# Kernel optimization log

Measured on AMD Instinct MI355X. Metric: run time of the kernel, lower is better.

The kernel has to match this reference:

```python
import jax, jax.numpy as jnp
import numpy as np

N_ENTITIES = 300000
N_ITEMS = 150000
N_USERS = 150000
N_EDGES = 2000000
N_INTER = 2000000
N_REL = 32
D = 64


def _scatter_mean(src, index, dim_size):
    # torch_scatter.scatter_mean: sum per segment divided by count; empty segments -> 0
    sums = jax.ops.segment_sum(src, index, num_segments=dim_size)
    cnt = jax.ops.segment_sum(jnp.ones((src.shape[0],), src.dtype), index, num_segments=dim_size)
    return sums / jnp.maximum(cnt, 1.0)[:, None]


def setup_inputs() -> dict:
    key = jax.random.key(0)
    ks = jax.random.split(key, 9)
    return {
        "entity_emb": jax.random.normal(ks[0], (N_ENTITIES, D), dtype=jnp.float32),
        "user_emb": jax.random.normal(ks[1], (N_USERS, D), dtype=jnp.float32),
        "edge_index": jax.random.randint(ks[2], (2, N_EDGES), 0, N_ENTITIES),
        "edge_type": jax.random.randint(ks[3], (N_EDGES,), 0, N_REL),
        "mat_row": jax.random.randint(ks[4], (N_INTER,), 0, N_USERS),
        "mat_col": jax.random.randint(ks[5], (N_INTER,), 0, N_ITEMS),
        "weight": jax.random.normal(ks[6], (N_REL, D), dtype=jnp.float32),
        "gate1_w": jax.random.normal(ks[7], (D, D), dtype=jnp.float32) * 0.1,
        "gate2_w": jax.random.normal(ks[8], (D, D), dtype=jnp.float32) * 0.1,
    }


def reference(entity_emb, user_emb, edge_index, edge_type, mat_row, mat_col, weight, gate1_w, gate2_w):
    head, tail = edge_index[0], edge_index[1]
    # KG aggregation: gather tail embeddings, modulate by relation emb, scatter-mean to head
    neigh_relation_emb = entity_emb[tail] * weight[edge_type]          # [E, D]
    entity_kg_agg = _scatter_mean(neigh_relation_emb, head, N_ENTITIES)
    item_kg_agg = entity_kg_agg[:N_ITEMS]                              # [I, D]
    att_kg_agg = entity_kg_agg[N_ITEMS:]                               # [Ent-I, D]
    # interaction aggregation: gather user emb by row, scatter-mean to item (col)
    item_int_agg = _scatter_mean(user_emb[mat_row], mat_col, N_ITEMS)  # [I, D]
    # gated fusion (F.linear: x @ W.T)
    gi = jax.nn.sigmoid(item_kg_agg @ gate1_w.T + item_int_agg @ gate2_w.T)
    item_emb_fusion = gi * item_kg_agg + (1.0 - gi) * item_int_agg
    # sparse mm with all-ones values == segment sum of fused item embs over users
    user_agg = jax.ops.segment_sum(item_emb_fusion[mat_col], mat_row, num_segments=N_USERS)
    final_entity_agg = jnp.concatenate([item_emb_fusion, att_kg_agg], axis=0)
    return (final_entity_agg, user_agg, item_kg_agg, item_int_agg)
```

## Files before the change

### kernel.cpp

```cpp
#include <hip/hip_runtime.h>

#define N_ENTITIES 300000
#define N_ITEMS    150000
#define N_USERS    150000
#define N_EDGES    2000000
#define N_INTER    2000000
#define D          64
#define N_TOT      (N_ENTITIES + N_ITEMS + N_USERS)

__global__ void hist_rank_kernel(const int* __restrict__ head,
                                 const int* __restrict__ mat_col,
                                 const int* __restrict__ mat_row,
                                 int* __restrict__ cnt,
                                 int* __restrict__ r_ent,
                                 int* __restrict__ r_item,
                                 int* __restrict__ r_user) {
    int e = blockIdx.x * 256 + threadIdx.x;
    if (e >= N_EDGES) return;
    int h = head[e], c = mat_col[e], r = mat_row[e];
    int a0 = atomicAdd(&cnt[h], 1);
    int a1 = atomicAdd(&cnt[N_ENTITIES + c], 1);
    int a2 = atomicAdd(&cnt[N_ENTITIES + N_ITEMS + r], 1);
    r_ent[e]  = a0;
    r_item[e] = a1;
    r_user[e] = a2;
}

__global__ void transpose_gates_kernel(const float* __restrict__ g1,
                                       const float* __restrict__ g2,
                                       float* __restrict__ g1t,
                                       float* __restrict__ g2t) {
    int i = blockIdx.x * 256 + threadIdx.x;
    if (i >= 64 * 64) return;
    int o = i >> 6, k = i & 63;
    g1t[k * 64 + o] = g1[i];
    g2t[k * 64 + o] = g2[i];
}

__global__ __launch_bounds__(256) void scan_partial(const int* __restrict__ in,
                                                    int* __restrict__ incl,
                                                    int* __restrict__ bsums,
                                                    int n) {
    __shared__ int lds[256];
    int t = threadIdx.x;
    int base = blockIdx.x * 1024 + t * 4;
    int v0 = (base + 0 < n) ? in[base + 0] : 0;
    int v1 = (base + 1 < n) ? in[base + 1] : 0;
    int v2 = (base + 2 < n) ? in[base + 2] : 0;
    int v3 = (base + 3 < n) ? in[base + 3] : 0;
    int s = v0 + v1 + v2 + v3;
    lds[t] = s;
    __syncthreads();
    for (int off = 1; off < 256; off <<= 1) {
        int x = (t >= off) ? lds[t - off] : 0;
        __syncthreads();
        lds[t] += x;
        __syncthreads();
    }
    int excl = lds[t] - s;
    if (base + 0 < n) incl[base + 0] = excl + v0;
    if (base + 1 < n) incl[base + 1] = excl + v0 + v1;
    if (base + 2 < n) incl[base + 2] = excl + v0 + v1 + v2;
    if (base + 3 < n) incl[base + 3] = excl + s;
    if (t == 255) bsums[blockIdx.x] = lds[255];
}

__global__ __launch_bounds__(1024) void scan_bsums(int* __restrict__ bsums, int nb) {
    __shared__ int lds[1024];
    int t = threadIdx.x;
    lds[t] = (t < nb) ? bsums[t] : 0;
    __syncthreads();
    for (int off = 1; off < 1024; off <<= 1) {
        int x = (t >= off) ? lds[t - off] : 0;
        __syncthreads();
        lds[t] += x;
        __syncthreads();
    }
    if (t < nb) bsums[t] = lds[t];
}

__global__ void scan_finalize(const int* __restrict__ incl,
                              const int* __restrict__ bsums,
                              int* __restrict__ off_ent,
                              int* __restrict__ off_item,
                              int* __restrict__ off_user) {
    int i = blockIdx.x * 256 + threadIdx.x;
    if (i >= N_TOT) return;
    int b = i >> 10;
    int g = incl[i] + ((b > 0) ? bsums[b - 1] : 0);
    if (i < N_ENTITIES) {
        off_ent[i + 1] = g;
        if (i == 0) { off_ent[0] = 0; }
    } else if (i < N_ENTITIES + N_ITEMS) {
        off_item[i - N_ENTITIES + 1] = g - N_EDGES;
        if (i == N_ENTITIES) { off_item[0] = 0; }
    } else {
        off_user[i - N_ENTITIES - N_ITEMS + 1] = g - 2 * N_EDGES;
        if (i == N_ENTITIES + N_ITEMS) { off_user[0] = 0; }
    }
}

__global__ void scatter_all_kernel(const int* __restrict__ head,
                                   const int* __restrict__ tail,
                                   const int* __restrict__ type,
                                   const int* __restrict__ mat_row,
                                   const int* __restrict__ mat_col,
                                   const int* __restrict__ r_ent,
                                   const int* __restrict__ r_item,
                                   const int* __restrict__ r_user,
                                   const int* __restrict__ off_ent,
                                   const int* __restrict__ off_item,
                                   const int* __restrict__ off_user,
                                   int* __restrict__ tt_sorted,
                                   int* __restrict__ row_sorted,
                                   int* __restrict__ col_sorted) {
    int e = blockIdx.x * 256 + threadIdx.x;
    if (e >= N_EDGES) return;
    int h = head[e], t = tail[e], ty = type[e];
    int r = mat_row[e], c = mat_col[e];
    tt_sorted[off_ent[h] + r_ent[e]]   = t | (ty << 19);
    row_sorted[off_item[c] + r_item[e]] = r;
    col_sorted[off_user[r] + r_user[e]] = c;
}

__global__ __launch_bounds__(256, 8) void agg_ent_kernel(
        const float* __restrict__ entity_emb, const float* __restrict__ weight,
        const int* __restrict__ off, const int* __restrict__ tt_sorted,
        float* __restrict__ out_item_kg, float* __restrict__ out_final) {
    int wave = threadIdx.x >> 6, lane = threadIdx.x & 63;
    int g = lane >> 4, q = lane & 15;
    int ent = blockIdx.x * 4 + wave;
    if (ent >= N_ENTITIES) return;
    int s = off[ent], e = off[ent + 1];
    int cnt = e - s;
    const float4* __restrict__ emb4 = (const float4*)entity_emb;
    const float4* __restrict__ wt4  = (const float4*)weight;
    float ax = 0.f, ay = 0.f, az = 0.f, aw = 0.f;
    for (int idx = s + g; idx < e; idx += 8) {
        int v0 = tt_sorted[idx];
        int i2 = idx + 4;
        bool p2 = (i2 < e);
        int v1 = p2 ? tt_sorted[i2] : 0;
        {
            int t = v0 & 0x7FFFF, w = v0 >> 19;
            float4 a = emb4[t * 16 + q];
            float4 b = wt4[w * 16 + q];
            ax += a.x * b.x; ay += a.y * b.y; az += a.z * b.z; aw += a.w * b.w;
        }
        if (p2) {
            int t = v1 & 0x7FFFF, w = v1 >> 19;
            float4 a = emb4[t * 16 + q];
            float4 b = wt4[w * 16 + q];
            ax += a.x * b.x; ay += a.y * b.y; az += a.z * b.z; aw += a.w * b.w;
        }
    }
    ax += __shfl_xor(ax, 16); ax += __shfl_xor(ax, 32);
    ay += __shfl_xor(ay, 16); ay += __shfl_xor(ay, 32);
    az += __shfl_xor(az, 16); az += __shfl_xor(az, 32);
    aw += __shfl_xor(aw, 16); aw += __shfl_xor(aw, 32);
    if (g == 0) {
        float inv = 1.0f / (float)(cnt > 1 ? cnt : 1);
        float4 r; r.x = ax * inv; r.y = ay * inv; r.z = az * inv; r.w = aw * inv;
        if (ent < N_ITEMS) ((float4*)out_item_kg)[ent * 16 + q] = r;
        else               ((float4*)out_final)[ent * 16 + q]   = r;
    }
}

__global__ __launch_bounds__(512, 6) void agg_item_fuse_kernel(
        const float* __restrict__ user_emb,
        const int* __restrict__ off, const int* __restrict__ row_sorted,
        const float* __restrict__ item_kg,
        const float* __restrict__ g1t, const float* __restrict__ g2t,
        float* __restrict__ out_item_int, float* __restrict__ out_final) {
    __shared__ float s_g1t[4096];
    __shared__ float s_g2t[4096];
    __shared__ float s_ii[8 * 64];

    {
        const float4* a = (const float4*)g1t;
        const float4* b = (const float4*)g2t;
        float4* sa = (float4*)s_g1t;
        float4* sb = (float4*)s_g2t;
        #pragma unroll
        for (int i = threadIdx.x; i < 1024; i += 512) { sa[i] = a[i]; sb[i] = b[i]; }
    }

    int wave = threadIdx.x >> 6, lane = threadIdx.x & 63;
    int g = lane >> 4, q = lane & 15;
    int item = blockIdx.x * 8 + wave;
    int s = off[item], e = off[item + 1];
    int cnt = e - s;
    const float4* __restrict__ ue4 = (const float4*)user_emb;
    float ax = 0.f, ay = 0.f, az = 0.f, aw = 0.f;
    for (int idx = s + g; idx < e; idx += 8) {
        int r0 = row_sorted[idx];
        int i2 = idx + 4;
        bool p2 = (i2 < e);
        int r1 = p2 ? row_sorted[i2] : 0;
        {
            float4 v = ue4[r0 * 16 + q];
            ax += v.x; ay += v.y; az += v.z; aw += v.w;
        }
        if (p2) {
            float4 v = ue4[r1 * 16 + q];
            ax += v.x; ay += v.y; az += v.z; aw += v.w;
        }
    }
    ax += __shfl_xor(ax, 16); ax += __shfl_xor(ax, 32);
    ay += __shfl_xor(ay, 16); ay += __shfl_xor(ay, 32);
    az += __shfl_xor(az, 16); az += __shfl_xor(az, 32);
    aw += __shfl_xor(aw, 16); aw += __shfl_xor(aw, 32);
    float inv = 1.0f / (float)(cnt > 1 ? cnt : 1);
    ax *= inv; ay *= inv; az *= inv; aw *= inv;
    if (g == 0) {
        float4 t; t.x = ax; t.y = ay; t.z = az; t.w = aw;
        *(float4*)&s_ii[wave * 64 + 4 * q] = t;
    }
    __syncthreads();

    const float* __restrict__ kgrow = item_kg + (long long)item * 64;
    float gx = 0.f, gy = 0.f, gz = 0.f, gw = 0.f;
    #pragma unroll 4
    for (int i = 0; i < 16; ++i) {
        int k = 16 * g + i;
        float kk = kgrow[k];
        float ik = s_ii[wave * 64 + k];
        float4 w1 = *(const float4*)&s_g1t[k * 64 + 4 * q];
        float4 w2 = *(const float4*)&s_g2t[k * 64 + 4 * q];
        gx += kk * w1.x + ik * w2.x;
        gy += kk * w1.y + ik * w2.y;
        gz += kk * w1.z + ik * w2.z;
        gw += kk * w1.w + ik * w2.w;
    }
    gx += __shfl_xor(gx, 16); gx += __shfl_xor(gx, 32);
    gy += __shfl_xor(gy, 16); gy += __shfl_xor(gy, 32);
    gz += __shfl_xor(gz, 16); gz += __shfl_xor(gz, 32);
    gw += __shfl_xor(gw, 16); gw += __shfl_xor(gw, 32);

    if (g == 0) {
        float4 kg4 = *(const float4*)&kgrow[4 * q];
        float4 ii4; ii4.x = ax; ii4.y = ay; ii4.z = az; ii4.w = aw;
        float4 o;
        float s0 = 1.0f / (1.0f + __expf(-gx)); o.x = s0 * kg4.x + (1.0f - s0) * ii4.x;
        float s1 = 1.0f / (1.0f + __expf(-gy)); o.y = s1 * kg4.y + (1.0f - s1) * ii4.y;
        float s2 = 1.0f / (1.0f + __expf(-gz)); o.z = s2 * kg4.z + (1.0f - s2) * ii4.z;
        float s3 = 1.0f / (1.0f + __expf(-gw)); o.w = s3 * kg4.w + (1.0f - s3) * ii4.w;
        ((float4*)out_item_int)[item * 16 + q] = ii4;
        ((float4*)out_final)[item * 16 + q]    = o;
    }
}

__global__ __launch_bounds__(256, 8) void agg_user_kernel(
        const float* __restrict__ fusion,
        const int* __restrict__ off, const int* __restrict__ col_sorted,
        float* __restrict__ out_user) {
    int wave = threadIdx.x >> 6, lane = threadIdx.x & 63;
    int g = lane >> 4, q = lane & 15;
    int user = blockIdx.x * 4 + wave;
    if (user >= N_USERS) return;
    int s = off[user], e = off[user + 1];
    const float4* __restrict__ f4 = (const float4*)fusion;
    float ax = 0.f, ay = 0.f, az = 0.f, aw = 0.f;
    for (int idx = s + g; idx < e; idx += 8) {
        int c0 = col_sorted[idx];
        int i2 = idx + 4;
        bool p2 = (i2 < e);
        int c1 = p2 ? col_sorted[i2] : 0;
        {
            float4 v = f4[c0 * 16 + q];
            ax += v.x; ay += v.y; az += v.z; aw += v.w;
        }
        if (p2) {
            float4 v = f4[c1 * 16 + q];
            ax += v.x; ay += v.y; az += v.z; aw += v.w;
        }
    }
    ax += __shfl_xor(ax, 16); ax += __shfl_xor(ax, 32);
    ay += __shfl_xor(ay, 16); ay += __shfl_xor(ay, 32);
    az += __shfl_xor(az, 16); az += __shfl_xor(az, 32);
    aw += __shfl_xor(aw, 16); aw += __shfl_xor(aw, 32);
    if (g == 0) {
        float4 r; r.x = ax; r.y = ay; r.z = az; r.w = aw;
        ((float4*)out_user)[user * 16 + q] = r;
    }
}


extern "C" void kernel_launch(void* const* d_in, const int* in_sizes, int n_in,
                              void* d_out, int out_size, void* d_ws, size_t ws_size,
                              hipStream_t stream) {
    const float* entity_emb = (const float*)d_in[0];
    const float* user_emb   = (const float*)d_in[1];
    const int*   edge_index = (const int*)d_in[2];
    const int*   edge_type  = (const int*)d_in[3];
    const int*   mat_row    = (const int*)d_in[4];
    const int*   mat_col    = (const int*)d_in[5];
    const float* weight     = (const float*)d_in[6];
    const float* g1         = (const float*)d_in[7];
    const float* g2         = (const float*)d_in[8];

    const int* edge_head = edge_index;
    const int* edge_tail = edge_index + N_EDGES;

    float* out = (float*)d_out;
    float* out_final    = out;
    float* out_user     = out + (long long)N_ENTITIES * D;
    float* out_item_kg  = out_user + (long long)N_USERS * D;
    float* out_item_int = out_item_kg + (long long)N_ITEMS * D;

    int* w = (int*)d_ws;
    float* g1t_glob = (float*)w;  w += 64 * 64;
    float* g2t_glob = (float*)w;  w += 64 * 64;
    int* cnt       = w;  w += N_TOT;
    int* off_ent   = w;  w += N_ENTITIES + 1;
    int* off_item  = w;  w += N_ITEMS + 1;
    int* off_user  = w;  w += N_USERS + 1;
    int* incl_tmp  = w;  w += N_TOT;
    int* bsums     = w;  w += 1024;
    int* r_ent     = w;  w += N_EDGES;
    int* r_item    = w;  w += N_INTER;
    int* r_user    = w;  w += N_INTER;
    int* tt_sorted = w;  w += N_EDGES;
    int* row_sorted= w;  w += N_INTER;
    int* col_sorted= w;  w += N_INTER;

    hipMemsetAsync(cnt, 0, (size_t)N_TOT * sizeof(int), stream);

    const int EB = (N_EDGES + 255) / 256;

    transpose_gates_kernel<<<16, 256, 0, stream>>>(g1, g2, g1t_glob, g2t_glob);

    hist_rank_kernel<<<EB, 256, 0, stream>>>(edge_head, mat_col, mat_row,
                                             cnt, r_ent, r_item, r_user);

    {
        int nb = (N_TOT + 1023) / 1024;
        scan_partial<<<nb, 256, 0, stream>>>(cnt, incl_tmp, bsums, N_TOT);
        scan_bsums<<<1, 1024, 0, stream>>>(bsums, nb);
        scan_finalize<<<(N_TOT + 255) / 256, 256, 0, stream>>>(
            incl_tmp, bsums, off_ent, off_item, off_user);
    }

    scatter_all_kernel<<<EB, 256, 0, stream>>>(
        edge_head, edge_tail, edge_type, mat_row, mat_col,
        r_ent, r_item, r_user, off_ent, off_item, off_user,
        tt_sorted, row_sorted, col_sorted);

    agg_ent_kernel<<<N_ENTITIES / 4, 256, 0, stream>>>(
        entity_emb, weight, off_ent, tt_sorted, out_item_kg, out_final);
    agg_item_fuse_kernel<<<N_ITEMS / 8, 512, 0, stream>>>(
        user_emb, off_item, row_sorted, out_item_kg, g1t_glob, g2t_glob,
        out_item_int, out_final);
    agg_user_kernel<<<N_USERS / 4, 256, 0, stream>>>(
        out_final, off_user, col_sorted, out_user);
}
```

Baseline: 1.027 ms.

## Privatize histogram counters per XCD to keep atomics local

Each XCD now atomically increments its own copy of the count array, selected by reading the hardware XCC id, instead of sharing one global array. This targets the cost of cross-die coherence traffic on atomics. The scan sums the eight copies, and a packed per-bin byte prefix tells the scatter where each XCD's slots begin. In exchange it adds eight times the memset and scan reads plus an extra prefix array. Packing offsets into 8 bits assumes no bin holds 256 or more items from one XCD.

```diff
diff --git a/kernel.cpp b/kernel.cpp
--- a/kernel.cpp
+++ b/kernel.cpp
@@ -7,23 +7,33 @@
 #define N_INTER    2000000
 #define D          64
 #define N_TOT      (N_ENTITIES + N_ITEMS + N_USERS)
+#define NXCD       8
+
+__device__ __forceinline__ int xcc_id() {
+    int x;
+    asm volatile("s_getreg_b32 %0, hwreg(HW_REG_XCC_ID)" : "=s"(x));
+    return x & (NXCD - 1);
+}
 
 __global__ void hist_rank_kernel(const int* __restrict__ head,
                                  const int* __restrict__ mat_col,
                                  const int* __restrict__ mat_row,
-                                 int* __restrict__ cnt,
+                                 int* __restrict__ cnt_x,
                                  int* __restrict__ r_ent,
                                  int* __restrict__ r_item,
                                  int* __restrict__ r_user) {
     int e = blockIdx.x * 256 + threadIdx.x;
     if (e >= N_EDGES) return;
+    int x = xcc_id();
+    int* __restrict__ mycnt = cnt_x + x * N_TOT;
+    int xt = x << 24;
     int h = head[e], c = mat_col[e], r = mat_row[e];
-    int a0 = atomicAdd(&cnt[h], 1);
-    int a1 = atomicAdd(&cnt[N_ENTITIES + c], 1);
-    int a2 = atomicAdd(&cnt[N_ENTITIES + N_ITEMS + r], 1);
-    r_ent[e]  = a0;
-    r_item[e] = a1;
-    r_user[e] = a2;
+    int a0 = atomicAdd(&mycnt[h], 1);
+    int a1 = atomicAdd(&mycnt[N_ENTITIES + c], 1);
+    int a2 = atomicAdd(&mycnt[N_ENTITIES + N_ITEMS + r], 1);
+    r_ent[e]  = a0 | xt;
+    r_item[e] = a1 | xt;
+    r_user[e] = a2 | xt;
 }
 
 __global__ void transpose_gates_kernel(const float* __restrict__ g1,
@@ -37,17 +47,22 @@
     g2t[k * 64 + o] = g2[i];
 }
 
-__global__ __launch_bounds__(256) void scan_partial(const int* __restrict__ in,
+__global__ __launch_bounds__(256) void scan_partial(const int* __restrict__ cnt_x,
                                                     int* __restrict__ incl,
                                                     int* __restrict__ bsums,
                                                     int n) {
     __shared__ int lds[256];
     int t = threadIdx.x;
     int base = blockIdx.x * 1024 + t * 4;
-    int v0 = (base + 0 < n) ? in[base + 0] : 0;
-    int v1 = (base + 1 < n) ? in[base + 1] : 0;
-    int v2 = (base + 2 < n) ? in[base + 2] : 0;
-    int v3 = (base + 3 < n) ? in[base + 3] : 0;
+    int v0 = 0, v1 = 0, v2 = 0, v3 = 0;
+    #pragma unroll
+    for (int x = 0; x < NXCD; ++x) {
+        const int* __restrict__ c = cnt_x + x * N_TOT;
+        if (base + 0 < n) v0 += c[base + 0];
+        if (base + 1 < n) v1 += c[base + 1];
+        if (base + 2 < n) v2 += c[base + 2];
+        if (base + 3 < n) v3 += c[base + 3];
+    }
     int s = v0 + v1 + v2 + v3;
     lds[t] = s;
     __syncthreads();
@@ -81,13 +96,27 @@
 
 __global__ void scan_finalize(const int* __restrict__ incl,
                               const int* __restrict__ bsums,
+                              const int* __restrict__ cnt_x,
                               int* __restrict__ off_ent,
                               int* __restrict__ off_item,
-                              int* __restrict__ off_user) {
+                              int* __restrict__ off_user,
+                              uint2* __restrict__ prefx) {
     int i = blockIdx.x * 256 + threadIdx.x;
     if (i >= N_TOT) return;
     int b = i >> 10;
     int g = incl[i] + ((b > 0) ? bsums[b - 1] : 0);
+
+    unsigned lo = 0, hi = 0;
+    int tot = 0;
+    #pragma unroll
+    for (int x = 0; x < NXCD; ++x) {
+        unsigned p = (unsigned)(tot & 0xFF);
+        if (x < 4) lo |= p << (8 * x);
+        else       hi |= p << (8 * (x - 4));
+        tot += cnt_x[x * N_TOT + i];
+    }
+    prefx[i] = make_uint2(lo, hi);
+
     if (i < N_ENTITIES) {
         off_ent[i + 1] = g;
         if (i == 0) { off_ent[0] = 0; }
@@ -98,6 +127,10 @@
         off_user[i - N_ENTITIES - N_ITEMS + 1] = g - 2 * N_EDGES;
         if (i == N_ENTITIES + N_ITEMS) { off_user[0] = 0; }
     }
+}
+
+__device__ __forceinline__ int pfx_get(uint2 p, int x) {
+    return (int)(((x < 4) ? (p.x >> (8 * x)) : (p.y >> (8 * (x - 4)))) & 0xFFu);
 }
 
 __global__ void scatter_all_kernel(const int* __restrict__ head,
@@ -111,6 +144,7 @@
                                    const int* __restrict__ off_ent,
                                    const int* __restrict__ off_item,
                                    const int* __restrict__ off_user,
+                                   const uint2* __restrict__ prefx,
                                    int* __restrict__ tt_sorted,
                                    int* __restrict__ row_sorted,
                                    int* __restrict__ col_sorted) {
@@ -118,9 +152,17 @@
     if (e >= N_EDGES) return;
     int h = head[e], t = tail[e], ty = type[e];
     int r = mat_row[e], c = mat_col[e];
-    tt_sorted[off_ent[h] + r_ent[e]]   = t | (ty << 19);
-    row_sorted[off_item[c] + r_item[e]] = r;
-    col_sorted[off_user[r] + r_user[e]] = c;
+
+    int v0 = r_ent[e];
+    int v1 = r_item[e];
+    int v2 = r_user[e];
+    int p0 = pfx_get(prefx[h], v0 >> 24);
+    int p1 = pfx_get(prefx[N_ENTITIES + c], v1 >> 24);
+    int p2 = pfx_get(prefx[N_ENTITIES + N_ITEMS + r], v2 >> 24);
+
+    tt_sorted[off_ent[h]  + p0 + (v0 & 0xFFFFFF)] = t | (ty << 19);
+    row_sorted[off_item[c] + p1 + (v1 & 0xFFFFFF)] = r;
+    col_sorted[off_user[r] + p2 + (v2 & 0xFFFFFF)] = c;
 }
 
 __global__ __launch_bounds__(256, 8) void agg_ent_kernel(
@@ -311,7 +353,8 @@
     int* w = (int*)d_ws;
     float* g1t_glob = (float*)w;  w += 64 * 64;
     float* g2t_glob = (float*)w;  w += 64 * 64;
-    int* cnt       = w;  w += N_TOT;
+    uint2* prefx    = (uint2*)w;  w += 2 * N_TOT;
+    int* cnt_x     = w;  w += NXCD * N_TOT;
     int* off_ent   = w;  w += N_ENTITIES + 1;
     int* off_item  = w;  w += N_ITEMS + 1;
     int* off_user  = w;  w += N_USERS + 1;
@@ -324,26 +367,26 @@
     int* row_sorted= w;  w += N_INTER;
     int* col_sorted= w;  w += N_INTER;
 
-    hipMemsetAsync(cnt, 0, (size_t)N_TOT * sizeof(int), stream);
+    hipMemsetAsync(cnt_x, 0, (size_t)NXCD * N_TOT * sizeof(int), stream);
 
     const int EB = (N_EDGES + 255) / 256;
 
     transpose_gates_kernel<<<16, 256, 0, stream>>>(g1, g2, g1t_glob, g2t_glob);
 
     hist_rank_kernel<<<EB, 256, 0, stream>>>(edge_head, mat_col, mat_row,
-                                             cnt, r_ent, r_item, r_user);
+                                             cnt_x, r_ent, r_item, r_user);
 
     {
         int nb = (N_TOT + 1023) / 1024;
-        scan_partial<<<nb, 256, 0, stream>>>(cnt, incl_tmp, bsums, N_TOT);
+        scan_partial<<<nb, 256, 0, stream>>>(cnt_x, incl_tmp, bsums, N_TOT);
         scan_bsums<<<1, 1024, 0, stream>>>(bsums, nb);
         scan_finalize<<<(N_TOT + 255) / 256, 256, 0, stream>>>(
-            incl_tmp, bsums, off_ent, off_item, off_user);
+            incl_tmp, bsums, cnt_x, off_ent, off_item, off_user, prefx);
     }
 
     scatter_all_kernel<<<EB, 256, 0, stream>>>(
         edge_head, edge_tail, edge_type, mat_row, mat_col,
-        r_ent, r_item, r_user, off_ent, off_item, off_user,
+        r_ent, r_item, r_user, off_ent, off_item, off_user, prefx,
         tt_sorted, row_sorted, col_sorted);
 
     agg_ent_kernel<<<N_ENTITIES / 4, 256, 0, stream>>>(
```

After: 1.072 ms. 4.4% more time.
